# Kernel tuning notes

Hardware: AMD Instinct MI355X
Metric: run time of the kernel (lower is better)

Reference implementation:

```python
import jax, jax.numpy as jnp
import numpy as np


def _graph_conv(x, src, dst, W_rel, b_rel, W_root):
    # PyG GraphConv (aggr='add'): out = lin_rel(sum_{j->i} x_j) + lin_root(x_i)
    agg = jax.ops.segment_sum(x[src], dst, num_segments=x.shape[0])  # [N, d]
    return agg @ W_rel + b_rel + x @ W_root


def setup_inputs() -> dict:
    N, E, D, H, G = 50000, 800000, 128, 128, 256
    key = jax.random.key(0)
    ks = jax.random.split(key, 24)
    x = jax.random.normal(ks[0], (N, D), dtype=jnp.float32)
    edge_index = jax.random.randint(ks[1], (2, E), 0, N, dtype=jnp.int64)
    batch = jnp.sort(jax.random.randint(ks[2], (N,), 0, G, dtype=jnp.int64))
    inp = {"x": x, "edge_index": edge_index, "batch": batch, "num_graphs": G}
    dims = [(D, H), (H, H), (H, H), (H, H), (H, H)]
    for i, (din, dout) in enumerate(dims, 1):
        s = 1.0 / np.sqrt(din)
        inp[f"W_rel{i}"] = jax.random.normal(ks[3 * i], (din, dout), dtype=jnp.float32) * s
        inp[f"b_rel{i}"] = jax.random.normal(ks[3 * i + 1], (dout,), dtype=jnp.float32) * s
        inp[f"W_root{i}"] = jax.random.normal(ks[3 * i + 2], (din, dout), dtype=jnp.float32) * s
    inp["fc1_W"] = jax.random.normal(ks[18], (H, H), dtype=jnp.float32) / np.sqrt(H)
    inp["fc1_b"] = jax.random.normal(ks[19], (H,), dtype=jnp.float32) / np.sqrt(H)
    inp["fc2_W"] = jax.random.normal(ks[20], (H, 1), dtype=jnp.float32) / np.sqrt(H)
    inp["fc2_b"] = jax.random.normal(ks[21], (1,), dtype=jnp.float32) / np.sqrt(H)
    return inp


def reference(x, edge_index, batch, num_graphs,
              W_rel1, b_rel1, W_root1,
              W_rel2, b_rel2, W_root2,
              W_rel3, b_rel3, W_root3,
              W_rel4, b_rel4, W_root4,
              W_rel5, b_rel5, W_root5,
              fc1_W, fc1_b, fc2_W, fc2_b):
    src, dst = edge_index[0], edge_index[1]
    h = x
    for Wr, br, Wl in ((W_rel1, b_rel1, W_root1), (W_rel2, b_rel2, W_root2),
                       (W_rel3, b_rel3, W_root3), (W_rel4, b_rel4, W_root4),
                       (W_rel5, b_rel5, W_root5)):
        h = jax.nn.relu(_graph_conv(h, src, dst, Wr, br, Wl))
    # global_add_pool -> [num_graphs, H]
    g = jax.ops.segment_sum(h, batch, num_segments=num_graphs)
    g = jax.nn.relu(g @ fc1_W + fc1_b)
    # dropout is identity in eval mode
    return g @ fc2_W + fc2_b  # [num_graphs, 1]
```

## Files before the change

### kernel.cpp

```cpp
#include <hip/hip_runtime.h>
#include <hip/hip_bf16.h>

typedef __attribute__((ext_vector_type(4))) float f32x4;
typedef __attribute__((ext_vector_type(8))) _Float16 f16x8;
typedef __attribute__((ext_vector_type(4))) _Float16 f16x4;

#define CHUNK 4096
#define BSH 7
#define CAP 4096
#define TM 32

__global__ __launch_bounds__(256) void cvt_kernel(const float* __restrict__ x,
                                                  _Float16* __restrict__ h, int total4) {
  int i = blockIdx.x * blockDim.x + threadIdx.x;
  if (i < total4) {
    float4 v = *(const float4*)(x + (size_t)i * 4);
    f16x4 o = {(_Float16)v.x, (_Float16)v.y, (_Float16)v.z, (_Float16)v.w};
    *(f16x4*)(h + (size_t)i * 4) = o;
  }
}

__global__ __launch_bounds__(256) void bhist_kernel(const int* __restrict__ dst,
                                                    int* __restrict__ gcnt, int E, int nb) {
  __shared__ int l[512];
  int t = threadIdx.x;
  for (int i = t; i < 512; i += 256) l[i] = 0;
  __syncthreads();
  int cbase = blockIdx.x * CHUNK;
  #pragma unroll
  for (int i = 0; i < CHUNK / 256; ++i) {
    int idx = cbase + i * 256 + t;
    if (idx < E) atomicAdd(&l[dst[idx] >> BSH], 1);
  }
  __syncthreads();
  for (int i = t; i < nb; i += 256) {
    int c = l[i];
    if (c) atomicAdd(&gcnt[i], c);
  }
}

__global__ __launch_bounds__(512) void bscan_kernel(const int* __restrict__ gcnt,
                                                    int* __restrict__ base,
                                                    int* __restrict__ gcursor, int nb, int E) {
  __shared__ int wsum[8], wpre[8];
  int t = threadIdx.x, lane = t & 63, w = t >> 6;
  int v = (t < nb) ? gcnt[t] : 0;
  int incl = v;
  #pragma unroll
  for (int o = 1; o < 64; o <<= 1) {
    int x = __shfl_up(incl, o, 64);
    if (lane >= o) incl += x;
  }
  if (lane == 63) wsum[w] = incl;
  __syncthreads();
  if (t == 0) {
    int run = 0;
    #pragma unroll
    for (int q = 0; q < 8; ++q) { wpre[q] = run; run += wsum[q]; }
  }
  __syncthreads();
  int excl = wpre[w] + incl - v;
  if (t < nb) { base[t] = excl; gcursor[t] = excl; }
  if (t == 0) base[nb] = E;
}

__global__ __launch_bounds__(256) void bscatter_kernel(const int* __restrict__ src,
                                                       const int* __restrict__ dst,
                                                       int* __restrict__ gcursor,
                                                       int2* __restrict__ pairs, int E, int nb) {
  __shared__ int lcnt[512], lstart[512], lpos[512], lgbase[512];
  __shared__ int2 lp[CHUNK];
  __shared__ int wsum[4], wpre[4];
  int t = threadIdx.x, lane = t & 63, w = t >> 6;
  for (int i = t; i < 512; i += 256) lcnt[i] = 0;
  __syncthreads();
  int cbase = blockIdx.x * CHUNK;
  int m = E - cbase; if (m > CHUNK) m = CHUNK;
  #pragma unroll
  for (int i = 0; i < CHUNK / 256; ++i) {
    int idx = i * 256 + t;
    if (idx < m) atomicAdd(&lcnt[dst[cbase + idx] >> BSH], 1);
  }
  __syncthreads();
  int c0 = lcnt[2 * t], c1 = lcnt[2 * t + 1];
  int s = c0 + c1, incl = s;
  #pragma unroll
  for (int o = 1; o < 64; o <<= 1) {
    int x = __shfl_up(incl, o, 64);
    if (lane >= o) incl += x;
  }
  if (lane == 63) wsum[w] = incl;
  __syncthreads();
  if (t == 0) {
    int run = 0;
    #pragma unroll
    for (int q = 0; q < 4; ++q) { wpre[q] = run; run += wsum[q]; }
  }
  __syncthreads();
  int excl = wpre[w] + incl - s;
  lstart[2 * t] = excl;          lpos[2 * t] = excl;
  lstart[2 * t + 1] = excl + c0; lpos[2 * t + 1] = excl + c0;
  if (2 * t < nb && c0 > 0) lgbase[2 * t] = atomicAdd(&gcursor[2 * t], c0);
  if (2 * t + 1 < nb && c1 > 0) lgbase[2 * t + 1] = atomicAdd(&gcursor[2 * t + 1], c1);
  __syncthreads();
  #pragma unroll
  for (int i = 0; i < CHUNK / 256; ++i) {
    int idx = i * 256 + t;
    if (idx < m) {
      int d = dst[cbase + idx], sv = src[cbase + idx];
      int p = atomicAdd(&lpos[d >> BSH], 1);
      lp[p] = make_int2(sv, d);
    }
  }
  __syncthreads();
  for (int i = t; i < m; i += 256) {
    int2 pr = lp[i];
    int b = pr.y >> BSH;
    pairs[lgbase[b] + (i - lstart[b])] = pr;
  }
}

__global__ __launch_bounds__(256) void bbuild_kernel(const int2* __restrict__ pairs,
                                                     const int* __restrict__ base,
                                                     int* __restrict__ row_ptr,
                                                     int* __restrict__ col, int N, int E) {
  __shared__ int cnt[128], cur[128], w2[2];
  __shared__ int cl[CAP];
  int b = blockIdx.x, t = threadIdx.x;
  int mb = base[b], me = base[b + 1], m = me - mb;
  if (t < 128) cnt[t] = 0;
  __syncthreads();
  for (int i = t; i < m; i += 256) atomicAdd(&cnt[pairs[mb + i].y & 127], 1);
  __syncthreads();
  int v = 0, incl = 0;
  if (t < 128) {
    v = cnt[t]; incl = v;
    #pragma unroll
    for (int o = 1; o < 64; o <<= 1) {
      int x = __shfl_up(incl, o, 64);
      if ((t & 63) >= o) incl += x;
    }
    if ((t & 63) == 63) w2[t >> 6] = incl;
  }
  __syncthreads();
  if (t < 128) {
    int excl = incl - v + ((t & 64) ? w2[0] : 0);
    cur[t] = excl;
    int node = (b << BSH) + t;
    if (node < N) row_ptr[node] = mb + excl;
  }
  if (b == 0 && t == 0) row_ptr[N] = E;
  __syncthreads();
  if (m <= CAP) {
    for (int i = t; i < m; i += 256) {
      int2 p = pairs[mb + i];
      int pos = atomicAdd(&cur[p.y & 127], 1);
      cl[pos] = p.x;
    }
    __syncthreads();
    for (int i = t; i < m; i += 256) col[mb + i] = cl[i];
  } else {
    for (int i = t; i < m; i += 256) {
      int2 p = pairs[mb + i];
      int pos = atomicAdd(&cur[p.y & 127], 1);
      col[mb + pos] = p.x;
    }
  }
}

__global__ void prep_kernel(const float* __restrict__ Wrel, const float* __restrict__ Wroot,
                            _Float16* __restrict__ Whi, _Float16* __restrict__ Wlo,
                            float wscale) {
  int idx = blockIdx.x * blockDim.x + threadIdx.x;
  int col = idx >> 8;
  int k = idx & 255;
  float v = (k < 128) ? Wrel[k * 128 + col] : Wroot[(k - 128) * 128 + col];
  v *= wscale;
  _Float16 hi = (_Float16)v;
  _Float16 lo = (_Float16)(v - (float)hi);
  Whi[idx] = hi;
  Wlo[idx] = lo;
}

__global__ __launch_bounds__(256) void gemm_fused(const _Float16* __restrict__ hin,
                                                  const int* __restrict__ row_ptr,
                                                  const int* __restrict__ col,
                                                  const _Float16* __restrict__ Whi,
                                                  const _Float16* __restrict__ Wlo,
                                                  const float* __restrict__ bias,
                                                  float bscale,
                                                  _Float16* __restrict__ out, int N) {
  __shared__ unsigned lds[TM * 64];
  const f16x8* __restrict__ hp = (const f16x8*)hin;
  int t = threadIdx.x, w = t >> 6, lane = t & 63;
  int g = lane >> 4, l16 = lane & 15;
  int row_base = blockIdx.x * TM;

  #pragma unroll
  for (int chunk = 0; chunk < 2; ++chunk) {
    int rl = w * 8 + chunk * 4 + g;
    int row = row_base + rl;
    float acc[8];
    #pragma unroll
    for (int q = 0; q < 8; ++q) acc[q] = 0.f;
    if (row < N) {
      int s = row_ptr[row], e = row_ptr[row + 1];
      if (s < e) {
        int c[8];
        #pragma unroll
        for (int q = 0; q < 8; ++q) { int idx = s + q; c[q] = col[idx < e ? idx : e - 1]; }
        int i = s;
        for (; i + 8 <= e; i += 8) {
          f16x8 v[8];
          #pragma unroll
          for (int q = 0; q < 8; ++q) v[q] = hp[(size_t)c[q] * 16 + l16];
          #pragma unroll
          for (int q = 0; q < 8; ++q) { int idx = i + 8 + q; c[q] = col[idx < e ? idx : e - 1]; }
          #pragma unroll
          for (int z = 0; z < 8; ++z)
            acc[z] += (((float)v[0][z] + (float)v[1][z]) + ((float)v[2][z] + (float)v[3][z])) +
                      (((float)v[4][z] + (float)v[5][z]) + ((float)v[6][z] + (float)v[7][z]));
        }
        if (i < e) {
          f16x8 v[8];
          #pragma unroll
          for (int q = 0; q < 8; ++q) v[q] = hp[(size_t)c[q] * 16 + l16];
          #pragma unroll
          for (int q = 0; q < 8; ++q) {
            float m = (i + q < e) ? 1.f : 0.f;
            #pragma unroll
            for (int z = 0; z < 8; ++z) acc[z] = fmaf(m, (float)v[q][z], acc[z]);
          }
        }
      }
    }
    f16x8 o;
    #pragma unroll
    for (int q = 0; q < 8; ++q) o[q] = (_Float16)acc[q];
    unsigned byte = (unsigned)(rl * 256 + l16 * 16) ^ (unsigned)((rl & 7) << 4);
    *(f16x8*)((char*)lds + byte) = o;
  }
  __syncthreads();

  int khalf = lane >> 4;
  int koff = khalf * 8;
  int col_base = w * 32;

  f32x4 acc[2][2];
  #pragma unroll
  for (int r = 0; r < 2; r++)
    #pragma unroll
    for (int c = 0; c < 2; c++) acc[r][c] = (f32x4){0.f, 0.f, 0.f, 0.f};

  #pragma unroll
  for (int ks = 0; ks < 8; ++ks) {
    int k0 = ks * 32;
    f16x8 bh[2], bl[2];
    #pragma unroll
    for (int c = 0; c < 2; c++) {
      int cc = col_base + c * 16 + l16;
      bh[c] = *(const f16x8*)(Whi + cc * 256 + k0 + koff);
      bl[c] = *(const f16x8*)(Wlo + cc * 256 + k0 + koff);
    }
    #pragma unroll
    for (int r = 0; r < 2; r++) {
      f16x8 a;
      if (ks < 4) {
        int arow = r * 16 + l16;
        unsigned byte = (unsigned)(arow * 256 + k0 * 2 + khalf * 16) ^ (unsigned)((arow & 7) << 4);
        a = *(const f16x8*)((const char*)lds + byte);
      } else {
        int row = row_base + r * 16 + l16;
        if (row >= N) row = N - 1;
        a = *(const f16x8*)(hin + (size_t)row * 128 + (k0 - 128) + koff);
      }
      #pragma unroll
      for (int c = 0; c < 2; c++) {
        acc[r][c] = __builtin_amdgcn_mfma_f32_16x16x32_f16(a, bh[c], acc[r][c], 0, 0, 0);
        acc[r][c] = __builtin_amdgcn_mfma_f32_16x16x32_f16(a, bl[c], acc[r][c], 0, 0, 0);
      }
    }
  }

  #pragma unroll
  for (int r = 0; r < 2; r++) {
    #pragma unroll
    for (int c = 0; c < 2; c++) {
      int cc = col_base + c * 16 + l16;
      float b = bias[cc] * bscale;
      #pragma unroll
      for (int tt = 0; tt < 4; tt++) {
        int row = row_base + r * 16 + khalf * 4 + tt;
        if (row < N) {
          float v = acc[r][c][tt] + b;
          out[(size_t)row * 128 + cc] = (_Float16)(v > 0.f ? v : 0.f);
        }
      }
    }
  }
}

static __device__ __forceinline__ int lbound(const int* __restrict__ a, int n, int v) {
  int lo = 0, hi = n;
  while (lo < hi) {
    int m = (lo + hi) >> 1;
    if (a[m] < v) lo = m + 1; else hi = m;
  }
  return lo;
}

__global__ __launch_bounds__(128) void poolhead_kernel(const _Float16* __restrict__ h,
                                                       const int* __restrict__ batch,
                                                       const float* __restrict__ fc1W,
                                                       const float* __restrict__ fc1b,
                                                       const float* __restrict__ fc2W,
                                                       const float* __restrict__ fc2b,
                                                       float* __restrict__ out, int N,
                                                       float unscale) {
  int gid = blockIdx.x, j = threadIdx.x;
  int start = lbound(batch, N, gid);
  int end = lbound(batch, N, gid + 1);
  float acc = 0.f;
  int r = start;
  for (; r + 3 < end; r += 4) {
    acc += (float)h[(size_t)r * 128 + j] + (float)h[(size_t)(r + 1) * 128 + j] +
           (float)h[(size_t)(r + 2) * 128 + j] + (float)h[(size_t)(r + 3) * 128 + j];
  }
  for (; r < end; ++r) acc += (float)h[(size_t)r * 128 + j];
  __shared__ float grow[128];
  __shared__ float red[128];
  grow[j] = acc * unscale;
  __syncthreads();
  float a1 = fc1b[j];
  #pragma unroll 8
  for (int k = 0; k < 128; ++k) a1 = fmaf(grow[k], fc1W[k * 128 + j], a1);
  a1 = a1 > 0.f ? a1 : 0.f;
  red[j] = a1 * fc2W[j];
  __syncthreads();
  #pragma unroll
  for (int s2 = 64; s2 > 0; s2 >>= 1) {
    if (j < s2) red[j] += red[j + s2];
    __syncthreads();
  }
  if (j == 0) out[gid] = red[0] + fc2b[0];
}

extern "C" void kernel_launch(void* const* d_in, const int* in_sizes, int n_in,
                              void* d_out, int out_size, void* d_ws, size_t ws_size,
                              hipStream_t stream) {
  const float* x = (const float*)d_in[0];
  const int* edge = (const int*)d_in[1];
  const int* batch = (const int*)d_in[2];
  const int N = in_sizes[0] / 128;
  const int E = in_sizes[1] / 2;
  const int G = out_size;
  const int* esrc = edge;
  const int* edst = edge + E;
  const int NB = (N + 127) >> BSH;

  char* ws = (char*)d_ws;
  size_t off = 0;
  auto alloc = [&](size_t bytes) -> void* {
    void* p = ws + off;
    off = (off + bytes + 255) & ~(size_t)255;
    return p;
  };
  _Float16* x16  = (_Float16*)alloc((size_t)N * 128 * 2);
  _Float16* bufA = (_Float16*)alloc((size_t)N * 128 * 2);
  _Float16* bufB = (_Float16*)alloc((size_t)N * 128 * 2);
  _Float16* Whi  = (_Float16*)alloc((size_t)5 * 32768 * 2);
  _Float16* Wlo  = (_Float16*)alloc((size_t)5 * 32768 * 2);
  int* row_ptr   = (int*)alloc((size_t)(N + 1) * 4);
  int* col       = (int*)alloc((size_t)E * 4);
  int2* pairs    = (int2*)alloc((size_t)E * 8);
  int* gcnt      = (int*)alloc(512 * 4);
  int* base      = (int*)alloc(520 * 4);
  int* gcursor   = (int*)alloc(512 * 4);
  if (off > ws_size) return;

  hipMemsetAsync(gcnt, 0, 512 * 4, stream);

  int nb1 = (E + CHUNK - 1) / CHUNK;
  bhist_kernel<<<nb1, 256, 0, stream>>>(edst, gcnt, E, NB);
  bscan_kernel<<<1, 512, 0, stream>>>(gcnt, base, gcursor, NB, E);
  bscatter_kernel<<<nb1, 256, 0, stream>>>(esrc, edst, gcursor, pairs, E, NB);
  bbuild_kernel<<<NB, 256, 0, stream>>>(pairs, base, row_ptr, col, N, E);

  cvt_kernel<<<(N * 128 / 4 + 255) / 256, 256, 0, stream>>>(x, x16, N * 128 / 4);

  const float S = 8.0f;
  float bscale = 1.0f;
  for (int l = 0; l < 5; ++l) {
    prep_kernel<<<128, 256, 0, stream>>>((const float*)d_in[4 + 3 * l],
                                         (const float*)d_in[6 + 3 * l],
                                         Whi + (size_t)l * 32768, Wlo + (size_t)l * 32768,
                                         1.0f / S);
  }

  const _Float16* hin = x16;
  _Float16* hout = bufA;
  int gemm_grid = (N + TM - 1) / TM;
  for (int l = 0; l < 5; ++l) {
    bscale /= S;
    gemm_fused<<<gemm_grid, 256, 0, stream>>>(hin, row_ptr, col,
                                              Whi + (size_t)l * 32768, Wlo + (size_t)l * 32768,
                                              (const float*)d_in[5 + 3 * l], bscale, hout, N);
    hin = hout;
    hout = (hout == bufA) ? bufB : bufA;
  }
  poolhead_kernel<<<G, 128, 0, stream>>>(hin, batch,
                                         (const float*)d_in[19], (const float*)d_in[20],
                                         (const float*)d_in[21], (const float*)d_in[22],
                                         (float*)d_out, N, 32768.0f);
}
```

Measured before the change: 383.4 us.

## Split fused gather-GEMM into separate SpMM and 64-row GEMM kernels

Splits the fused aggregation+GEMM kernel into a standalone SpMM kernel, which writes the fp16 neighbour sum to a new global buffer, and a GEMM kernel with 64-row tiles that reads aggregated and root features straight from global memory. The five weight-prep launches are merged into one launch. The aim is to let the latency-bound gather run at full occupancy with small blocks, free of the LDS and MFMA register pressure, while the GEMM gets more reuse per weight load. The cost is an extra N×128 fp16 round trip through global memory per layer and twice as many launches in the layer loop.

```diff
diff --git a/kernel.cpp b/kernel.cpp
--- a/kernel.cpp
+++ b/kernel.cpp
@@ -8,7 +8,6 @@
 #define CHUNK 4096
 #define BSH 7
 #define CAP 4096
-#define TM 32
 
 __global__ __launch_bounds__(256) void cvt_kernel(const float* __restrict__ x,
                                                   _Float16* __restrict__ h, int total4) {
@@ -168,112 +167,109 @@
   }
 }
 
-__global__ void prep_kernel(const float* __restrict__ Wrel, const float* __restrict__ Wroot,
-                            _Float16* __restrict__ Whi, _Float16* __restrict__ Wlo,
-                            float wscale) {
-  int idx = blockIdx.x * blockDim.x + threadIdx.x;
+struct W10 { const float* p[10]; };
+
+__global__ __launch_bounds__(256) void prep_kernel(W10 wp, _Float16* __restrict__ Whi,
+                                                   _Float16* __restrict__ Wlo, float wscale) {
+  int l = blockIdx.x >> 7;
+  int idx = (blockIdx.x & 127) * 256 + threadIdx.x;
   int col = idx >> 8;
   int k = idx & 255;
+  const float* __restrict__ Wrel = wp.p[l];
+  const float* __restrict__ Wroot = wp.p[5 + l];
   float v = (k < 128) ? Wrel[k * 128 + col] : Wroot[(k - 128) * 128 + col];
   v *= wscale;
   _Float16 hi = (_Float16)v;
   _Float16 lo = (_Float16)(v - (float)hi);
-  Whi[idx] = hi;
-  Wlo[idx] = lo;
-}
-
-__global__ __launch_bounds__(256) void gemm_fused(const _Float16* __restrict__ hin,
-                                                  const int* __restrict__ row_ptr,
-                                                  const int* __restrict__ col,
-                                                  const _Float16* __restrict__ Whi,
-                                                  const _Float16* __restrict__ Wlo,
-                                                  const float* __restrict__ bias,
-                                                  float bscale,
-                                                  _Float16* __restrict__ out, int N) {
-  __shared__ unsigned lds[TM * 64];
-  const f16x8* __restrict__ hp = (const f16x8*)hin;
-  int t = threadIdx.x, w = t >> 6, lane = t & 63;
-  int g = lane >> 4, l16 = lane & 15;
-  int row_base = blockIdx.x * TM;
-
-  #pragma unroll
-  for (int chunk = 0; chunk < 2; ++chunk) {
-    int rl = w * 8 + chunk * 4 + g;
-    int row = row_base + rl;
-    float acc[8];
-    #pragma unroll
-    for (int q = 0; q < 8; ++q) acc[q] = 0.f;
-    if (row < N) {
-      int s = row_ptr[row], e = row_ptr[row + 1];
-      if (s < e) {
-        int c[8];
+  Whi[(size_t)l * 32768 + idx] = hi;
+  Wlo[(size_t)l * 32768 + idx] = lo;
+}
+
+__global__ __launch_bounds__(256) void spmm_kernel(const _Float16* __restrict__ hin,
+                                                   const int* __restrict__ row_ptr,
+                                                   const int* __restrict__ col,
+                                                   _Float16* __restrict__ agg, int N) {
+  int t = threadIdx.x;
+  int grp = t >> 4, l16 = t & 15;
+  int row = blockIdx.x * 16 + grp;
+  if (row >= N) return;
+  const char* __restrict__ hb = (const char*)hin;
+  unsigned lofs = (unsigned)l16 << 4;
+  int s = row_ptr[row], e = row_ptr[row + 1];
+  float acc[8];
+  #pragma unroll
+  for (int q = 0; q < 8; ++q) acc[q] = 0.f;
+  if (s < e) {
+    int c[8];
+    #pragma unroll
+    for (int q = 0; q < 8; ++q) { int x = s + q; c[q] = col[x < e ? x : e - 1]; }
+    int i = s;
+    for (; i + 8 <= e; i += 8) {
+      f16x8 v[8];
+      #pragma unroll
+      for (int q = 0; q < 8; ++q) v[q] = *(const f16x8*)(hb + ((((unsigned)c[q]) << 8) | lofs));
+      #pragma unroll
+      for (int q = 0; q < 8; ++q) { int x = i + 8 + q; c[q] = col[x < e ? x : e - 1]; }
+      #pragma unroll
+      for (int z = 0; z < 8; ++z)
+        acc[z] += (((float)v[0][z] + (float)v[1][z]) + ((float)v[2][z] + (float)v[3][z])) +
+                  (((float)v[4][z] + (float)v[5][z]) + ((float)v[6][z] + (float)v[7][z]));
+    }
+    if (i < e) {
+      f16x8 v[8];
+      #pragma unroll
+      for (int q = 0; q < 8; ++q) v[q] = *(const f16x8*)(hb + ((((unsigned)c[q]) << 8) | lofs));
+      #pragma unroll
+      for (int q = 0; q < 8; ++q) {
+        float m = (i + q < e) ? 1.f : 0.f;
         #pragma unroll
-        for (int q = 0; q < 8; ++q) { int idx = s + q; c[q] = col[idx < e ? idx : e - 1]; }
-        int i = s;
-        for (; i + 8 <= e; i += 8) {
-          f16x8 v[8];
-          #pragma unroll
-          for (int q = 0; q < 8; ++q) v[q] = hp[(size_t)c[q] * 16 + l16];
-          #pragma unroll
-          for (int q = 0; q < 8; ++q) { int idx = i + 8 + q; c[q] = col[idx < e ? idx : e - 1]; }
-          #pragma unroll
-          for (int z = 0; z < 8; ++z)
-            acc[z] += (((float)v[0][z] + (float)v[1][z]) + ((float)v[2][z] + (float)v[3][z])) +
-                      (((float)v[4][z] + (float)v[5][z]) + ((float)v[6][z] + (float)v[7][z]));
-        }
-        if (i < e) {
-          f16x8 v[8];
-          #pragma unroll
-          for (int q = 0; q < 8; ++q) v[q] = hp[(size_t)c[q] * 16 + l16];
-          #pragma unroll
-          for (int q = 0; q < 8; ++q) {
-            float m = (i + q < e) ? 1.f : 0.f;
-            #pragma unroll
-            for (int z = 0; z < 8; ++z) acc[z] = fmaf(m, (float)v[q][z], acc[z]);
-          }
-        }
+        for (int z = 0; z < 8; ++z) acc[z] = fmaf(m, (float)v[q][z], acc[z]);
       }
     }
-    f16x8 o;
-    #pragma unroll
-    for (int q = 0; q < 8; ++q) o[q] = (_Float16)acc[q];
-    unsigned byte = (unsigned)(rl * 256 + l16 * 16) ^ (unsigned)((rl & 7) << 4);
-    *(f16x8*)((char*)lds + byte) = o;
-  }
-  __syncthreads();
-
+  }
+  f16x8 o;
+  #pragma unroll
+  for (int q = 0; q < 8; ++q) o[q] = (_Float16)acc[q];
+  *(f16x8*)(agg + (size_t)row * 128 + l16 * 8) = o;
+}
+
+__global__ __launch_bounds__(256) void gemm_kernel(const _Float16* __restrict__ Aagg,
+                                                   const _Float16* __restrict__ Ah,
+                                                   const _Float16* __restrict__ Whi,
+                                                   const _Float16* __restrict__ Wlo,
+                                                   const float* __restrict__ bias,
+                                                   float bscale,
+                                                   _Float16* __restrict__ out, int N) {
+  int wv = threadIdx.x >> 6;
+  int lane = threadIdx.x & 63;
+  int l16 = lane & 15;
   int khalf = lane >> 4;
   int koff = khalf * 8;
-  int col_base = w * 32;
-
-  f32x4 acc[2][2];
-  #pragma unroll
-  for (int r = 0; r < 2; r++)
+  int row_base = blockIdx.x * 64;
+  int col_base = wv * 32;
+
+  f32x4 acc[4][2];
+  #pragma unroll
+  for (int r = 0; r < 4; r++)
     #pragma unroll
     for (int c = 0; c < 2; c++) acc[r][c] = (f32x4){0.f, 0.f, 0.f, 0.f};
 
   #pragma unroll
   for (int ks = 0; ks < 8; ++ks) {
     int k0 = ks * 32;
+    const _Float16* Abase = (ks < 4) ? (Aagg + k0) : (Ah + (k0 - 128));
     f16x8 bh[2], bl[2];
     #pragma unroll
     for (int c = 0; c < 2; c++) {
-      int cc = col_base + c * 16 + l16;
-      bh[c] = *(const f16x8*)(Whi + cc * 256 + k0 + koff);
-      bl[c] = *(const f16x8*)(Wlo + cc * 256 + k0 + koff);
-    }
-    #pragma unroll
-    for (int r = 0; r < 2; r++) {
-      f16x8 a;
-      if (ks < 4) {
-        int arow = r * 16 + l16;
-        unsigned byte = (unsigned)(arow * 256 + k0 * 2 + khalf * 16) ^ (unsigned)((arow & 7) << 4);
-        a = *(const f16x8*)((const char*)lds + byte);
-      } else {
-        int row = row_base + r * 16 + l16;
-        if (row >= N) row = N - 1;
-        a = *(const f16x8*)(hin + (size_t)row * 128 + (k0 - 128) + koff);
-      }
+      int col = col_base + c * 16 + l16;
+      bh[c] = *(const f16x8*)(Whi + col * 256 + k0 + koff);
+      bl[c] = *(const f16x8*)(Wlo + col * 256 + k0 + koff);
+    }
+    #pragma unroll
+    for (int r = 0; r < 4; r++) {
+      int row = row_base + r * 16 + l16;
+      if (row >= N) row = N - 1;
+      f16x8 a = *(const f16x8*)(Abase + (size_t)row * 128 + koff);
       #pragma unroll
       for (int c = 0; c < 2; c++) {
         acc[r][c] = __builtin_amdgcn_mfma_f32_16x16x32_f16(a, bh[c], acc[r][c], 0, 0, 0);
@@ -283,17 +279,17 @@
   }
 
   #pragma unroll
-  for (int r = 0; r < 2; r++) {
+  for (int r = 0; r < 4; r++) {
     #pragma unroll
     for (int c = 0; c < 2; c++) {
-      int cc = col_base + c * 16 + l16;
-      float b = bias[cc] * bscale;
+      int col = col_base + c * 16 + l16;
+      float b = bias[col] * bscale;
       #pragma unroll
       for (int tt = 0; tt < 4; tt++) {
         int row = row_base + r * 16 + khalf * 4 + tt;
         if (row < N) {
           float v = acc[r][c][tt] + b;
-          out[(size_t)row * 128 + cc] = (_Float16)(v > 0.f ? v : 0.f);
+          out[(size_t)row * 128 + col] = (_Float16)(v > 0.f ? v : 0.f);
         }
       }
     }
@@ -368,6 +364,7 @@
   _Float16* x16  = (_Float16*)alloc((size_t)N * 128 * 2);
   _Float16* bufA = (_Float16*)alloc((size_t)N * 128 * 2);
   _Float16* bufB = (_Float16*)alloc((size_t)N * 128 * 2);
+  _Float16* agg  = (_Float16*)alloc((size_t)N * 128 * 2);
   _Float16* Whi  = (_Float16*)alloc((size_t)5 * 32768 * 2);
   _Float16* Wlo  = (_Float16*)alloc((size_t)5 * 32768 * 2);
   int* row_ptr   = (int*)alloc((size_t)(N + 1) * 4);
@@ -389,22 +386,24 @@
   cvt_kernel<<<(N * 128 / 4 + 255) / 256, 256, 0, stream>>>(x, x16, N * 128 / 4);
 
   const float S = 8.0f;
+  W10 wp;
+  for (int l = 0; l < 5; ++l) {
+    wp.p[l] = (const float*)d_in[4 + 3 * l];
+    wp.p[5 + l] = (const float*)d_in[6 + 3 * l];
+  }
+  prep_kernel<<<640, 256, 0, stream>>>(wp, Whi, Wlo, 1.0f / S);
+
+  const _Float16* hin = x16;
+  _Float16* hout = bufA;
+  int spmm_grid = (N + 15) / 16;
+  int gemm_grid = (N + 63) / 64;
   float bscale = 1.0f;
   for (int l = 0; l < 5; ++l) {
-    prep_kernel<<<128, 256, 0, stream>>>((const float*)d_in[4 + 3 * l],
-                                         (const float*)d_in[6 + 3 * l],
-                                         Whi + (size_t)l * 32768, Wlo + (size_t)l * 32768,
-                                         1.0f / S);
-  }
-
-  const _Float16* hin = x16;
-  _Float16* hout = bufA;
-  int gemm_grid = (N + TM - 1) / TM;
-  for (int l = 0; l < 5; ++l) {
     bscale /= S;
-    gemm_fused<<<gemm_grid, 256, 0, stream>>>(hin, row_ptr, col,
-                                              Whi + (size_t)l * 32768, Wlo + (size_t)l * 32768,
-                                              (const float*)d_in[5 + 3 * l], bscale, hout, N);
+    spmm_kernel<<<spmm_grid, 256, 0, stream>>>(hin, row_ptr, col, agg, N);
+    gemm_kernel<<<gemm_grid, 256, 0, stream>>>(agg, hin,
+                                               Whi + (size_t)l * 32768, Wlo + (size_t)l * 32768,
+                                               (const float*)d_in[5 + 3 * l], bscale, hout, N);
     hin = hout;
     hout = (hout == bufA) ? bufB : bufA;
   }
```

New measurement: 374.4 us. 2.3% less time.
